# Performance work log

Hardware: AMD Instinct MI355X
Metric: run time of the kernel (lower is better)

Reference implementation:

```python
import jax, jax.numpy as jnp
import numpy as np
from jax import lax

T, B, INPUT, HID, OUT, FUT = 128, 1024, 4, 512, 4, 32


def setup_inputs() -> dict:
    key = jax.random.key(0)
    ks = jax.random.split(key, 12)
    s = 0.05  # small init like uniform(-1/sqrt(H), 1/sqrt(H))
    inp = {
        "x": jax.random.normal(ks[0], (T, B, INPUT), jnp.float32),
        "Wih1": jax.random.normal(ks[1], (4 * HID, INPUT), jnp.float32) * s,
        "Whh1": jax.random.normal(ks[2], (4 * HID, HID), jnp.float32) * s,
        "bih1": jax.random.normal(ks[3], (4 * HID,), jnp.float32) * s,
        "bhh1": jax.random.normal(ks[4], (4 * HID,), jnp.float32) * s,
        "Wih2": jax.random.normal(ks[5], (4 * HID, HID), jnp.float32) * s,
        "Whh2": jax.random.normal(ks[6], (4 * HID, HID), jnp.float32) * s,
        "bih2": jax.random.normal(ks[7], (4 * HID,), jnp.float32) * s,
        "bhh2": jax.random.normal(ks[8], (4 * HID,), jnp.float32) * s,
        "Wl": jax.random.normal(ks[9], (OUT, HID), jnp.float32) * s,
        "bl": jax.random.normal(ks[10], (OUT,), jnp.float32) * s,
        "future": FUT,
    }
    return inp


def _cell(xt, h, c, Wih, Whh, bih, bhh):
    # PyTorch LSTMCell gate order: i, f, g, o
    g = xt @ Wih.T + bih + h @ Whh.T + bhh  # [B, 4H]
    i, f, gg, o = jnp.split(g, 4, axis=-1)
    c = jax.nn.sigmoid(f) * c + jax.nn.sigmoid(i) * jnp.tanh(gg)
    h = jax.nn.sigmoid(o) * jnp.tanh(c)
    return h, c


def reference(x, Wih1, Whh1, bih1, bhh1, Wih2, Whh2, bih2, bhh2, Wl, bl, future):
    nb = x.shape[1]
    H = Whh1.shape[1]
    z = jnp.zeros((nb, H), x.dtype)

    def step1(carry, xt):
        h1, c1, h2, c2 = carry
        h1, c1 = _cell(xt, h1, c1, Wih1, Whh1, bih1, bhh1)
        h2, c2 = _cell(h1, h2, c2, Wih2, Whh2, bih2, bhh2)
        return (h1, c1, h2, c2), None

    (h1, c1, h2, c2), _ = lax.scan(step1, (z, z, z, z), x)
    tmp_out = h2  # frozen last hidden of cell 2 (faithful to original bug)

    def step2(carry, _):
        h1, c1, h2, c2 = carry
        # original future loop reuses lstm2 weights for both updates
        h1, c1 = _cell(tmp_out, h1, c1, Wih2, Whh2, bih2, bhh2)
        h2, c2 = _cell(h1, h2, c2, Wih2, Whh2, bih2, bhh2)
        out = h2 @ Wl.T + bl  # [B, OUT]
        return (h1, c1, h2, c2), out

    _, outs = lax.scan(step2, (h1, c1, h2, c2), None, length=future)
    return outs  # [future, B, OUT]
```

## Files before the change

kernel.cpp:

```cpp
#include <hip/hip_runtime.h>

typedef _Float16 v8h __attribute__((ext_vector_type(8)));
typedef float v4f __attribute__((ext_vector_type(4)));
typedef unsigned int uint;

#define OFF_BAR   0
#define OFF_AO0   4096
#define OFF_AO1   (OFF_AO0 + (1<<21))
#define OFF_AF0   (OFF_AO1 + (1<<21))
#define OFF_AF1   (OFF_AF0 + (1<<21))
#define OFF_W1    (OFF_AF1 + (1<<21))
#define OFF_W2    (OFF_W1 + (1<<21))
#define OFF_B1    (OFF_W2 + (1<<22))
#define OFF_B2    (OFF_B1 + 8192)

__global__ __launch_bounds__(256, 1)
void lstm_prep(const float* __restrict__ Whh1, const float* __restrict__ Wih2,
               const float* __restrict__ Whh2, const float* __restrict__ bih1,
               const float* __restrict__ bhh1, const float* __restrict__ bih2,
               const float* __restrict__ bhh2,
               _Float16* __restrict__ W1p, _Float16* __restrict__ W2p,
               float* __restrict__ bs1, float* __restrict__ bs2)
{
  const int total = 1048576 + 2097152 + 4096;
  for (int i = blockIdx.x*blockDim.x + threadIdx.x; i < total; i += gridDim.x*blockDim.x) {
    if (i < 1048576) {
      int nt = i >> 13, rem = i & 8191;
      int k32 = rem >> 9, c = rem & 511;
      int lane = c >> 3, el = c & 7;
      int n = nt*16 + (lane & 15);
      int k = k32*32 + (lane >> 4)*8 + el;
      W1p[i] = (_Float16)Whh1[n*512 + k];
    } else if (i < 3145728) {
      int j = i - 1048576;
      int nt = j >> 14, rem = j & 16383;
      int k32 = rem >> 9, c = rem & 511;
      int lane = c >> 3, el = c & 7;
      int n = nt*16 + (lane & 15);
      int k = k32*32 + (lane >> 4)*8 + el;
      float v = (k < 512) ? Wih2[n*512 + k] : Whh2[n*512 + (k - 512)];
      W2p[j] = (_Float16)v;
    } else {
      int n = i - 3145728;
      if (n < 2048) bs1[n] = bih1[n] + bhh1[n];
      else          bs2[n-2048] = bih2[n-2048] + bhh2[n-2048];
    }
  }
}

__device__ __forceinline__ float sigmoidf_(float z) { return 1.f / (1.f + __expf(-z)); }
__device__ __forceinline__ float tanhf_(float z)    { return 1.f - 2.f/(1.f + __expf(2.f*z)); }

__device__ __forceinline__ v8h ld_frag_dev(const _Float16* base, uint off) {
  union { unsigned long long u[2]; v8h h; } cv;
  const unsigned long long* q = (const unsigned long long*)(base + off);
  cv.u[0] = __hip_atomic_load(q,     __ATOMIC_RELAXED, __HIP_MEMORY_SCOPE_AGENT);
  cv.u[1] = __hip_atomic_load(q + 1, __ATOMIC_RELAXED, __HIP_MEMORY_SCOPE_AGENT);
  return cv.h;
}

__global__ __launch_bounds__(256, 2)
void lstm_main(const float* __restrict__ x, const float* __restrict__ Wih1,
               const float* __restrict__ Wl, const float* __restrict__ blv,
               _Float16* __restrict__ AO0, _Float16* __restrict__ AO1,
               _Float16* __restrict__ AF0, _Float16* __restrict__ AF1,
               const _Float16* __restrict__ W1, const _Float16* __restrict__ W2,
               const float* __restrict__ bs1, const float* __restrict__ bs2,
               int* __restrict__ bar, float* __restrict__ out)
{
  __shared__ float lred[14336];
  const int tid  = threadIdx.x;
  const int wv   = tid >> 6, lane = tid & 63;
  const int quad = lane >> 4, lc = lane & 15;
  const int kh   = wv >> 1;
  const int cw   = (wv & 1) ^ kh;
  const int bid  = blockIdx.x;
  const int jg   = bid >> 3;
  const int ht   = (bid & 7)*2 + (jg & 1);
  const int bt   = jg >> 1;

  _Float16* const AOv[2] = {AO0, AO1};
  _Float16* const AFv[2] = {AF0, AF1};

  const int erow = tid >> 3, enib = tid & 7;
  const int tid2  = tid - 128;
  const int b_loc = (tid2 >= 0) ? (tid2 >> 2) : 0, oct = tid2 & 3;
  const int m     = b_loc & 15, mtile_e = bt*2 + (b_loc >> 4);
  const int STASH = 8448;

  int ntg_[8];
  #pragma unroll
  for (int tt = 0; tt < 8; tt++) ntg_[tt] = (tt>>1)*32 + ht*2 + (tt&1);

  float c1s[4], c2s[4];
  #pragma unroll
  for (int i = 0; i < 4; i++) { c1s[i] = 0.f; c2s[i] = 0.f; }

  for (int r = 0; r < 162; r++) {
    const bool p1 = r < 129;
    const int  f  = r - 129;
    const int  wp = p1 ? (r & 1) : (f & 1);
    const int  rp = wp ^ 1;
    const _Float16* A1 = p1 ? AOv[rp] : AFv[rp];
    const _Float16* A2 = AOv[rp];
    const bool skip1 = (r == 128 || r == 161);
    const bool skip2 = (r == 0   || r == 129);

    const _Float16* Ac = cw ? A2 : A1;
    const _Float16* Bc = cw ? W2 : (p1 ? W1 : W2);
    const int wk   = cw ? 32 : (p1 ? 16 : 32);
    const int half = cw ? 16 : (p1 ? 8 : 16);
    const int ch0  = kh * half;

    v4f acc[2][8];
    #pragma unroll
    for (int i2 = 0; i2 < 2; i2++)
      #pragma unroll
      for (int tt = 0; tt < 8; tt++) acc[i2][tt] = (v4f){0,0,0,0};

    uint aoff[2];
    #pragma unroll
    for (int i2 = 0; i2 < 2; i2++)
      aoff[i2] = (uint)(((bt*2 + i2)*32 + ch0)*512 + lane*8);
    uint boff[8];
    #pragma unroll
    for (int tt = 0; tt < 8; tt++)
      boff[tt] = (uint)((ntg_[tt]*wk + ch0)*512 + lane*8);

    #pragma unroll 4
    for (int cc = 0; cc < half; cc++) {
      v8h av[2];
      #pragma unroll
      for (int i2 = 0; i2 < 2; i2++)
        av[i2] = ld_frag_dev(Ac, aoff[i2] + cc*512);
      #pragma unroll
      for (int tt = 0; tt < 8; tt++) {
        v8h bv = *(const v8h*)(Bc + boff[tt] + cc*512);
        #pragma unroll
        for (int i2 = 0; i2 < 2; i2++)
          acc[i2][tt] = __builtin_amdgcn_mfma_f32_16x16x32_f16(av[i2], bv, acc[i2][tt], 0, 0, 0);
      }
    }

    const int rbase = cw * 4096;
    if (kh) {
      #pragma unroll
      for (int i2 = 0; i2 < 2; i2++)
        #pragma unroll
        for (int tt = 0; tt < 8; tt++)
          *(v4f*)&lred[rbase + ((i2*8 + tt)*64 + lane)*4] = acc[i2][tt];
    }
    __syncthreads();
    if (!kh) {
      #pragma unroll
      for (int i2 = 0; i2 < 2; i2++)
        #pragma unroll
        for (int tt = 0; tt < 8; tt++)
          acc[i2][tt] += *(const v4f*)&lred[rbase + ((i2*8 + tt)*64 + lane)*4];
    }
    __syncthreads();

    if (!kh && cw == 0) {
      #pragma unroll
      for (int i2 = 0; i2 < 2; i2++)
        #pragma unroll
        for (int tt = 0; tt < 8; tt++) {
          int row = i2*16 + quad*4;
          int col = tt*16 + lc;
          #pragma unroll
          for (int rr = 0; rr < 4; rr++) lred[(row + rr)*132 + col] = acc[i2][tt][rr];
        }
    }
    __syncthreads();

    {
      const float* bsx = p1 ? bs1 : bs2;
      float g[4][4];
      #pragma unroll
      for (int g4 = 0; g4 < 4; g4++) {
        v4f gv = *(const v4f*)&lred[erow*132 + g4*32 + enib*4];
        v4f bv = *(const v4f*)&bsx[g4*512 + ht*32 + enib*4];
        #pragma unroll
        for (int j = 0; j < 4; j++) g[g4][j] = gv[j] + bv[j];
      }
      if (p1 && r < 128) {
        const v4f xv = *(const v4f*)(x + ((size_t)r*1024 + bt*32 + erow)*4);
        #pragma unroll
        for (int g4 = 0; g4 < 4; g4++)
          #pragma unroll
          for (int j = 0; j < 4; j++) {
            int hh = ht*32 + enib*4 + j;
            const v4f w = *(const v4f*)(Wih1 + (size_t)(g4*512 + hh)*4);
            g[g4][j] += xv[0]*w[0] + xv[1]*w[1] + xv[2]*w[2] + xv[3]*w[3];
          }
      }
      if (!skip1) {
        v4f hf;
        #pragma unroll
        for (int j = 0; j < 4; j++) {
          float ig = sigmoidf_(g[0][j]), fg = sigmoidf_(g[1][j]);
          float gg = tanhf_(g[2][j]),    og = sigmoidf_(g[3][j]);
          float c = fg*c1s[j] + ig*gg;
          c1s[j] = c;
          hf[j] = og * tanhf_(c);
        }
        *(v4f*)&lred[STASH + erow*36 + enib*4] = hf;
      }
    }
    __syncthreads();

    if (tid >= 128 && !skip1) {
      v4f h0 = *(const v4f*)&lred[STASH + b_loc*36 + oct*8];
      v4f h1 = *(const v4f*)&lred[STASH + b_loc*36 + oct*8 + 4];
      union { _Float16 h8[8]; unsigned long long u[2]; } hu;
      #pragma unroll
      for (int j = 0; j < 4; j++) { hu.h8[j] = (_Float16)h0[j]; hu.h8[4+j] = (_Float16)h1[j]; }
      auto st16 = [&](_Float16* bp, int chunk) {
        unsigned long long* p = (unsigned long long*)
          (bp + (((size_t)(mtile_e*32 + chunk)) << 9) + (oct*16 + m)*8);
        __hip_atomic_store(p,     hu.u[0], __ATOMIC_RELAXED, __HIP_MEMORY_SCOPE_AGENT);
        __hip_atomic_store(p + 1, hu.u[1], __ATOMIC_RELAXED, __HIP_MEMORY_SCOPE_AGENT);
      };
      if (p1) {
        st16(AOv[wp], ht);
        if (r == 127) st16(AFv[1], 16 + ht);
      } else {
        st16(AFv[wp], 16 + ht);
        st16(AOv[wp], ht);
      }
    }
    if (!kh && cw == 1) {
      #pragma unroll
      for (int i2 = 0; i2 < 2; i2++)
        #pragma unroll
        for (int tt = 0; tt < 8; tt++) {
          int row = i2*16 + quad*4;
          int col = tt*16 + lc;
          #pragma unroll
          for (int rr = 0; rr < 4; rr++) lred[(row + rr)*132 + col] = acc[i2][tt][rr];
        }
    }
    __syncthreads();

    {
      float g[4][4];
      #pragma unroll
      for (int g4 = 0; g4 < 4; g4++) {
        v4f gv = *(const v4f*)&lred[erow*132 + g4*32 + enib*4];
        v4f bv = *(const v4f*)&bs2[g4*512 + ht*32 + enib*4];
        #pragma unroll
        for (int j = 0; j < 4; j++) g[g4][j] = gv[j] + bv[j];
      }
      if (!skip2) {
        v4f hf;
        #pragma unroll
        for (int j = 0; j < 4; j++) {
          float ig = sigmoidf_(g[0][j]), fg = sigmoidf_(g[1][j]);
          float gg = tanhf_(g[2][j]),    og = sigmoidf_(g[3][j]);
          float c = fg*c2s[j] + ig*gg;
          c2s[j] = c;
          hf[j] = og * tanhf_(c);
        }
        *(v4f*)&lred[STASH + erow*36 + enib*4] = hf;
      }
    }
    __syncthreads();

    if (tid >= 128 && !skip2) {
      v4f h0 = *(const v4f*)&lred[STASH + b_loc*36 + oct*8];
      v4f h1 = *(const v4f*)&lred[STASH + b_loc*36 + oct*8 + 4];
      union { _Float16 h8[8]; unsigned long long u[2]; } hu;
      #pragma unroll
      for (int j = 0; j < 4; j++) { hu.h8[j] = (_Float16)h0[j]; hu.h8[4+j] = (_Float16)h1[j]; }
      auto st16 = [&](_Float16* bp, int chunk) {
        unsigned long long* p = (unsigned long long*)
          (bp + (((size_t)(mtile_e*32 + chunk)) << 9) + (oct*16 + m)*8);
        __hip_atomic_store(p,     hu.u[0], __ATOMIC_RELAXED, __HIP_MEMORY_SCOPE_AGENT);
        __hip_atomic_store(p + 1, hu.u[1], __ATOMIC_RELAXED, __HIP_MEMORY_SCOPE_AGENT);
      };
      st16(AOv[wp], 16 + ht);
      if (r == 128) { st16(AFv[0], ht); st16(AFv[1], ht); }
    }
    if (tid < 128 && !p1 && r >= 130) {
      const int s = r - 130;
      int bb = tid >> 2, o = tid & 3;
      float sa = (ht == 0) ? blv[o] : 0.f;
      const float* wl = Wl + (size_t)o*512 + ht*32;
      #pragma unroll
      for (int jj = 0; jj < 32; jj++) sa += lred[STASH + bb*36 + jj] * wl[jj];
      atomicAdd(&out[(((size_t)s*1024) + bt*32 + bb)*4 + o], sa);
    }
    __syncthreads();

    if (tid == 0) {
      int* ctr = bar + bt*32;
      __hip_atomic_fetch_add(ctr, 1, __ATOMIC_RELAXED, __HIP_MEMORY_SCOPE_AGENT);
      const int target = 16*(r+1);
      while (__hip_atomic_load(ctr, __ATOMIC_RELAXED, __HIP_MEMORY_SCOPE_AGENT) < target)
        __builtin_amdgcn_s_sleep(1);
    }
    __syncthreads();
  }
}

extern "C" void kernel_launch(void* const* d_in, const int* in_sizes, int n_in,
                              void* d_out, int out_size, void* d_ws, size_t ws_size,
                              hipStream_t stream) {
  const float* x    = (const float*)d_in[0];
  const float* Wih1 = (const float*)d_in[1];
  const float* Whh1 = (const float*)d_in[2];
  const float* bih1 = (const float*)d_in[3];
  const float* bhh1 = (const float*)d_in[4];
  const float* Wih2 = (const float*)d_in[5];
  const float* Whh2 = (const float*)d_in[6];
  const float* bih2 = (const float*)d_in[7];
  const float* bhh2 = (const float*)d_in[8];
  const float* Wl   = (const float*)d_in[9];
  const float* bl   = (const float*)d_in[10];

  char* ws = (char*)d_ws;
  int*      bar = (int*)(ws + OFF_BAR);
  _Float16* AO0 = (_Float16*)(ws + OFF_AO0);
  _Float16* AO1 = (_Float16*)(ws + OFF_AO1);
  _Float16* AF0 = (_Float16*)(ws + OFF_AF0);
  _Float16* AF1 = (_Float16*)(ws + OFF_AF1);
  _Float16* W1p = (_Float16*)(ws + OFF_W1);
  _Float16* W2p = (_Float16*)(ws + OFF_W2);
  float*    bs1 = (float*)(ws + OFF_B1);
  float*    bs2 = (float*)(ws + OFF_B2);

  hipMemsetAsync(ws, 0, (size_t)OFF_W1, stream);
  hipMemsetAsync(d_out, 0, (size_t)out_size * sizeof(float), stream);

  lstm_prep<<<2048, 256, 0, stream>>>(Whh1, Wih2, Whh2, bih1, bhh1, bih2, bhh2,
                                      W1p, W2p, bs1, bs2);
  lstm_main<<<512, 256, 0, stream>>>(x, Wih1, Wl, bl, AO0, AO1, AF0, AF1,
                                     W1p, W2p, bs1, bs2, bar, (float*)d_out);
}
```

Baseline: 2.916 ms.

## Software-pipeline A-fragment loads and signal barrier before output projection

Replaces the inner GEMM loop with a templated, fully unrolled version. It prefetches up to eight K-chunks of the recurrent A fragments into registers ahead of use, to hide global/L2 latency on the atomic loads. It also moves the barrier arrival to before the output-projection atomicAdd work, so other blocks can proceed while this block computes its output contribution. The cost is higher register pressure from the prefetch buffer, which may reduce occupancy or cause spills.

```diff
diff --git a/kernel.cpp b/kernel.cpp
--- a/kernel.cpp
+++ b/kernel.cpp
@@ -59,6 +59,36 @@
   return cv.h;
 }
 
+template<int HALF>
+__device__ __forceinline__ void gemm_k(const _Float16* __restrict__ Ac,
+                                       const _Float16* __restrict__ Bc,
+                                       const uint* aoff, const uint* boff,
+                                       v4f (&acc)[2][8])
+{
+  constexpr int PF = (HALF < 8) ? HALF : 8;
+  v8h apf[PF][2];
+  #pragma unroll
+  for (int s = 0; s < PF; s++) {
+    apf[s][0] = ld_frag_dev(Ac, aoff[0] + s*512);
+    apf[s][1] = ld_frag_dev(Ac, aoff[1] + s*512);
+  }
+  #pragma unroll
+  for (int cc = 0; cc < HALF; cc++) {
+    v8h av0 = apf[cc % PF][0];
+    v8h av1 = apf[cc % PF][1];
+    if (cc + PF < HALF) {
+      apf[cc % PF][0] = ld_frag_dev(Ac, aoff[0] + (cc + PF)*512);
+      apf[cc % PF][1] = ld_frag_dev(Ac, aoff[1] + (cc + PF)*512);
+    }
+    #pragma unroll
+    for (int tt = 0; tt < 8; tt++) {
+      v8h bv = *(const v8h*)(Bc + boff[tt] + cc*512);
+      acc[0][tt] = __builtin_amdgcn_mfma_f32_16x16x32_f16(av0, bv, acc[0][tt], 0, 0, 0);
+      acc[1][tt] = __builtin_amdgcn_mfma_f32_16x16x32_f16(av1, bv, acc[1][tt], 0, 0, 0);
+    }
+  }
+}
+
 __global__ __launch_bounds__(256, 2)
 void lstm_main(const float* __restrict__ x, const float* __restrict__ Wih1,
                const float* __restrict__ Wl, const float* __restrict__ blv,
@@ -127,20 +157,8 @@
     for (int tt = 0; tt < 8; tt++)
       boff[tt] = (uint)((ntg_[tt]*wk + ch0)*512 + lane*8);
 
-    #pragma unroll 4
-    for (int cc = 0; cc < half; cc++) {
-      v8h av[2];
-      #pragma unroll
-      for (int i2 = 0; i2 < 2; i2++)
-        av[i2] = ld_frag_dev(Ac, aoff[i2] + cc*512);
-      #pragma unroll
-      for (int tt = 0; tt < 8; tt++) {
-        v8h bv = *(const v8h*)(Bc + boff[tt] + cc*512);
-        #pragma unroll
-        for (int i2 = 0; i2 < 2; i2++)
-          acc[i2][tt] = __builtin_amdgcn_mfma_f32_16x16x32_f16(av[i2], bv, acc[i2][tt], 0, 0, 0);
-      }
-    }
+    if (half == 8) gemm_k<8>(Ac, Bc, aoff, boff, acc);
+    else           gemm_k<16>(Ac, Bc, aoff, boff, acc);
 
     const int rbase = cw * 4096;
     if (kh) {
@@ -281,6 +299,12 @@
       st16(AOv[wp], 16 + ht);
       if (r == 128) { st16(AFv[0], ht); st16(AFv[1], ht); }
     }
+    __syncthreads();
+
+    if (tid == 0) {
+      int* ctr = bar + bt*32;
+      __hip_atomic_fetch_add(ctr, 1, __ATOMIC_RELAXED, __HIP_MEMORY_SCOPE_AGENT);
+    }
     if (tid < 128 && !p1 && r >= 130) {
       const int s = r - 130;
       int bb = tid >> 2, o = tid & 3;
@@ -290,11 +314,8 @@
       for (int jj = 0; jj < 32; jj++) sa += lred[STASH + bb*36 + jj] * wl[jj];
       atomicAdd(&out[(((size_t)s*1024) + bt*32 + bb)*4 + o], sa);
     }
-    __syncthreads();
-
     if (tid == 0) {
       int* ctr = bar + bt*32;
-      __hip_atomic_fetch_add(ctr, 1, __ATOMIC_RELAXED, __HIP_MEMORY_SCOPE_AGENT);
       const int target = 16*(r+1);
       while (__hip_atomic_load(ctr, __ATOMIC_RELAXED, __HIP_MEMORY_SCOPE_AGENT) < target)
         __builtin_amdgcn_s_sleep(1);
```

After: 3.624 ms. 24.3% more time.

## Process both LSTM cells' epilogues concurrently with split thread halves

Applied to the files above, without the earlier changes.

The split-K reduction now adds partial sums straight into the gate tiles in shared memory, so the separate reduction buffer pass goes away. Both cells' gate tiles (cw 0 and 1) are written to separate regions. The two halves of the block then run the cell-1 and cell-2 nonlinearities in parallel, each thread handling 8 hidden units. This removes several __syncthreads barriers and serialized epilogue phases per step, in exchange for more registers per thread (8 cell states, g[4][8]) and a larger shared footprint.

```diff
diff --git a/kernel.cpp b/kernel.cpp
--- a/kernel.cpp
+++ b/kernel.cpp
@@ -50,6 +50,7 @@
 
 __device__ __forceinline__ float sigmoidf_(float z) { return 1.f / (1.f + __expf(-z)); }
 __device__ __forceinline__ float tanhf_(float z)    { return 1.f - 2.f/(1.f + __expf(2.f*z)); }
+__device__ __forceinline__ float dot4_(v4f a, v4f b){ return a[0]*b[0]+a[1]*b[1]+a[2]*b[2]+a[3]*b[3]; }
 
 __device__ __forceinline__ v8h ld_frag_dev(const _Float16* base, uint off) {
   union { unsigned long long u[2]; v8h h; } cv;
@@ -82,19 +83,22 @@
   _Float16* const AOv[2] = {AO0, AO1};
   _Float16* const AFv[2] = {AF0, AF1};
 
-  const int erow = tid >> 3, enib = tid & 7;
+  const int half2 = tid >> 7;
+  const int et    = tid & 127;
+  const int erow2 = et >> 2;
+  const int ecg   = et & 3;
   const int tid2  = tid - 128;
   const int b_loc = (tid2 >= 0) ? (tid2 >> 2) : 0, oct = tid2 & 3;
   const int m     = b_loc & 15, mtile_e = bt*2 + (b_loc >> 4);
-  const int STASH = 8448;
+  const int GR1 = 0, GR2 = 4224, ST1 = 8448, ST2 = 9600;
 
   int ntg_[8];
   #pragma unroll
   for (int tt = 0; tt < 8; tt++) ntg_[tt] = (tt>>1)*32 + ht*2 + (tt&1);
 
-  float c1s[4], c2s[4];
+  float cs[8];
   #pragma unroll
-  for (int i = 0; i < 4; i++) { c1s[i] = 0.f; c2s[i] = 0.f; }
+  for (int i = 0; i < 8; i++) cs[i] = 0.f;
 
   for (int r = 0; r < 162; r++) {
     const bool p1 = r < 129;
@@ -142,25 +146,8 @@
       }
     }
 
-    const int rbase = cw * 4096;
+    const int gbase = cw ? GR2 : GR1;
     if (kh) {
-      #pragma unroll
-      for (int i2 = 0; i2 < 2; i2++)
-        #pragma unroll
-        for (int tt = 0; tt < 8; tt++)
-          *(v4f*)&lred[rbase + ((i2*8 + tt)*64 + lane)*4] = acc[i2][tt];
-    }
-    __syncthreads();
-    if (!kh) {
-      #pragma unroll
-      for (int i2 = 0; i2 < 2; i2++)
-        #pragma unroll
-        for (int tt = 0; tt < 8; tt++)
-          acc[i2][tt] += *(const v4f*)&lred[rbase + ((i2*8 + tt)*64 + lane)*4];
-    }
-    __syncthreads();
-
-    if (!kh && cw == 0) {
       #pragma unroll
       for (int i2 = 0; i2 < 2; i2++)
         #pragma unroll
@@ -168,118 +155,100 @@
           int row = i2*16 + quad*4;
           int col = tt*16 + lc;
           #pragma unroll
-          for (int rr = 0; rr < 4; rr++) lred[(row + rr)*132 + col] = acc[i2][tt][rr];
+          for (int rr = 0; rr < 4; rr++) lred[(row + rr)*132 + gbase + col] = acc[i2][tt][rr];
         }
     }
     __syncthreads();
 
+    if (!kh) {
+      #pragma unroll
+      for (int i2 = 0; i2 < 2; i2++)
+        #pragma unroll
+        for (int tt = 0; tt < 8; tt++) {
+          int row = i2*16 + quad*4;
+          int col = tt*16 + lc;
+          #pragma unroll
+          for (int rr = 0; rr < 4; rr++) {
+            int p = (row + rr)*132 + gbase + col;
+            lred[p] = acc[i2][tt][rr] + lred[p];
+          }
+        }
+    }
+    __syncthreads();
+
     {
-      const float* bsx = p1 ? bs1 : bs2;
-      float g[4][4];
+      const int gb = half2 ? GR2 : GR1;
+      const int sb = half2 ? ST2 : ST1;
+      const float* bsx = half2 ? bs2 : (p1 ? bs1 : bs2);
+      const bool skipc = half2 ? skip2 : skip1;
+      const bool xterm = (half2 == 0) && p1 && (r < 128);
+      float g[4][8];
       #pragma unroll
       for (int g4 = 0; g4 < 4; g4++) {
-        v4f gv = *(const v4f*)&lred[erow*132 + g4*32 + enib*4];
-        v4f bv = *(const v4f*)&bsx[g4*512 + ht*32 + enib*4];
-        #pragma unroll
-        for (int j = 0; j < 4; j++) g[g4][j] = gv[j] + bv[j];
-      }
-      if (p1 && r < 128) {
-        const v4f xv = *(const v4f*)(x + ((size_t)r*1024 + bt*32 + erow)*4);
+        v4f a0 = *(const v4f*)&lred[gb + erow2*132 + g4*32 + ecg*8];
+        v4f a1 = *(const v4f*)&lred[gb + erow2*132 + g4*32 + ecg*8 + 4];
+        v4f b0 = *(const v4f*)&bsx[g4*512 + ht*32 + ecg*8];
+        v4f b1 = *(const v4f*)&bsx[g4*512 + ht*32 + ecg*8 + 4];
+        #pragma unroll
+        for (int j = 0; j < 4; j++) { g[g4][j] = a0[j] + b0[j]; g[g4][4+j] = a1[j] + b1[j]; }
+      }
+      if (xterm) {
+        const v4f xv = *(const v4f*)(x + ((size_t)r*1024 + bt*32 + erow2)*4);
         #pragma unroll
         for (int g4 = 0; g4 < 4; g4++)
           #pragma unroll
-          for (int j = 0; j < 4; j++) {
-            int hh = ht*32 + enib*4 + j;
+          for (int j = 0; j < 8; j++) {
+            int hh = ht*32 + ecg*8 + j;
             const v4f w = *(const v4f*)(Wih1 + (size_t)(g4*512 + hh)*4);
-            g[g4][j] += xv[0]*w[0] + xv[1]*w[1] + xv[2]*w[2] + xv[3]*w[3];
+            g[g4][j] += dot4_(xv, w);
           }
       }
-      if (!skip1) {
-        v4f hf;
-        #pragma unroll
-        for (int j = 0; j < 4; j++) {
+      if (!skipc) {
+        v4f h0, h1v;
+        #pragma unroll
+        for (int j = 0; j < 8; j++) {
           float ig = sigmoidf_(g[0][j]), fg = sigmoidf_(g[1][j]);
           float gg = tanhf_(g[2][j]),    og = sigmoidf_(g[3][j]);
-          float c = fg*c1s[j] + ig*gg;
-          c1s[j] = c;
-          hf[j] = og * tanhf_(c);
+          float c = fg*cs[j] + ig*gg;
+          cs[j] = c;
+          float hv = og * tanhf_(c);
+          if (j < 4) h0[j] = hv; else h1v[j-4] = hv;
         }
-        *(v4f*)&lred[STASH + erow*36 + enib*4] = hf;
-      }
-    }
-    __syncthreads();
-
-    if (tid >= 128 && !skip1) {
-      v4f h0 = *(const v4f*)&lred[STASH + b_loc*36 + oct*8];
-      v4f h1 = *(const v4f*)&lred[STASH + b_loc*36 + oct*8 + 4];
+        *(v4f*)&lred[sb + erow2*36 + ecg*8]     = h0;
+        *(v4f*)&lred[sb + erow2*36 + ecg*8 + 4] = h1v;
+      }
+    }
+    __syncthreads();
+
+    if (tid >= 128) {
       union { _Float16 h8[8]; unsigned long long u[2]; } hu;
-      #pragma unroll
-      for (int j = 0; j < 4; j++) { hu.h8[j] = (_Float16)h0[j]; hu.h8[4+j] = (_Float16)h1[j]; }
       auto st16 = [&](_Float16* bp, int chunk) {
         unsigned long long* p = (unsigned long long*)
           (bp + (((size_t)(mtile_e*32 + chunk)) << 9) + (oct*16 + m)*8);
         __hip_atomic_store(p,     hu.u[0], __ATOMIC_RELAXED, __HIP_MEMORY_SCOPE_AGENT);
         __hip_atomic_store(p + 1, hu.u[1], __ATOMIC_RELAXED, __HIP_MEMORY_SCOPE_AGENT);
       };
-      if (p1) {
-        st16(AOv[wp], ht);
-        if (r == 127) st16(AFv[1], 16 + ht);
-      } else {
-        st16(AFv[wp], 16 + ht);
-        st16(AOv[wp], ht);
-      }
-    }
-    if (!kh && cw == 1) {
-      #pragma unroll
-      for (int i2 = 0; i2 < 2; i2++)
-        #pragma unroll
-        for (int tt = 0; tt < 8; tt++) {
-          int row = i2*16 + quad*4;
-          int col = tt*16 + lc;
-          #pragma unroll
-          for (int rr = 0; rr < 4; rr++) lred[(row + rr)*132 + col] = acc[i2][tt][rr];
+      if (!skip1) {
+        v4f h0 = *(const v4f*)&lred[ST1 + b_loc*36 + oct*8];
+        v4f h1v = *(const v4f*)&lred[ST1 + b_loc*36 + oct*8 + 4];
+        #pragma unroll
+        for (int j = 0; j < 4; j++) { hu.h8[j] = (_Float16)h0[j]; hu.h8[4+j] = (_Float16)h1v[j]; }
+        if (p1) {
+          st16(AOv[wp], ht);
+          if (r == 127) st16(AFv[1], 16 + ht);
+        } else {
+          st16(AFv[wp], 16 + ht);
+          st16(AOv[wp], ht);
         }
-    }
-    __syncthreads();
-
-    {
-      float g[4][4];
-      #pragma unroll
-      for (int g4 = 0; g4 < 4; g4++) {
-        v4f gv = *(const v4f*)&lred[erow*132 + g4*32 + enib*4];
-        v4f bv = *(const v4f*)&bs2[g4*512 + ht*32 + enib*4];
-        #pragma unroll
-        for (int j = 0; j < 4; j++) g[g4][j] = gv[j] + bv[j];
       }
       if (!skip2) {
-        v4f hf;
-        #pragma unroll
-        for (int j = 0; j < 4; j++) {
-          float ig = sigmoidf_(g[0][j]), fg = sigmoidf_(g[1][j]);
-          float gg = tanhf_(g[2][j]),    og = sigmoidf_(g[3][j]);
-          float c = fg*c2s[j] + ig*gg;
-          c2s[j] = c;
-          hf[j] = og * tanhf_(c);
-        }
-        *(v4f*)&lred[STASH + erow*36 + enib*4] = hf;
-      }
-    }
-    __syncthreads();
-
-    if (tid >= 128 && !skip2) {
-      v4f h0 = *(const v4f*)&lred[STASH + b_loc*36 + oct*8];
-      v4f h1 = *(const v4f*)&lred[STASH + b_loc*36 + oct*8 + 4];
-      union { _Float16 h8[8]; unsigned long long u[2]; } hu;
-      #pragma unroll
-      for (int j = 0; j < 4; j++) { hu.h8[j] = (_Float16)h0[j]; hu.h8[4+j] = (_Float16)h1[j]; }
-      auto st16 = [&](_Float16* bp, int chunk) {
-        unsigned long long* p = (unsigned long long*)
-          (bp + (((size_t)(mtile_e*32 + chunk)) << 9) + (oct*16 + m)*8);
-        __hip_atomic_store(p,     hu.u[0], __ATOMIC_RELAXED, __HIP_MEMORY_SCOPE_AGENT);
-        __hip_atomic_store(p + 1, hu.u[1], __ATOMIC_RELAXED, __HIP_MEMORY_SCOPE_AGENT);
-      };
-      st16(AOv[wp], 16 + ht);
-      if (r == 128) { st16(AFv[0], ht); st16(AFv[1], ht); }
+        v4f h0 = *(const v4f*)&lred[ST2 + b_loc*36 + oct*8];
+        v4f h1v = *(const v4f*)&lred[ST2 + b_loc*36 + oct*8 + 4];
+        #pragma unroll
+        for (int j = 0; j < 4; j++) { hu.h8[j] = (_Float16)h0[j]; hu.h8[4+j] = (_Float16)h1v[j]; }
+        st16(AOv[wp], 16 + ht);
+        if (r == 128) { st16(AFv[0], ht); st16(AFv[1], ht); }
+      }
     }
     if (tid < 128 && !p1 && r >= 130) {
       const int s = r - 130;
@@ -287,7 +256,7 @@
       float sa = (ht == 0) ? blv[o] : 0.f;
       const float* wl = Wl + (size_t)o*512 + ht*32;
       #pragma unroll
-      for (int jj = 0; jj < 32; jj++) sa += lred[STASH + bb*36 + jj] * wl[jj];
+      for (int jj = 0; jj < 32; jj++) sa += lred[ST2 + bb*36 + jj] * wl[jj];
       atomicAdd(&out[(((size_t)s*1024) + bt*32 + bb)*4 + o], sa);
     }
     __syncthreads();
```

Result: slower. 3.101 ms (+6.3%).

## Split hidden tiles in half and run twice as many persistent blocks

Applied to the files above, without the earlier changes.

Each block now computes 16 hidden units (4 gate n-tiles) instead of 32. The grid grows from 512 to 1024 blocks, with launch bounds raised to 4 blocks per CU and LDS shrunk so they stay co-resident. The aim is to shorten the per-step MFMA and weight-load chain on the recurrent critical path. The cost is that each block reloads the same activation fragments, and the software grid barrier now waits on 32 blocks per batch tile instead of 16. It also relies on all 1024 blocks being resident at once.

```diff
diff --git a/kernel.cpp b/kernel.cpp
--- a/kernel.cpp
+++ b/kernel.cpp
@@ -50,6 +50,7 @@
 
 __device__ __forceinline__ float sigmoidf_(float z) { return 1.f / (1.f + __expf(-z)); }
 __device__ __forceinline__ float tanhf_(float z)    { return 1.f - 2.f/(1.f + __expf(2.f*z)); }
+__device__ __forceinline__ float dot4_(v4f a, v4f b){ return a[0]*b[0]+a[1]*b[1]+a[2]*b[2]+a[3]*b[3]; }
 
 __device__ __forceinline__ v8h ld_frag_dev(const _Float16* base, uint off) {
   union { unsigned long long u[2]; v8h h; } cv;
@@ -59,7 +60,7 @@
   return cv.h;
 }
 
-__global__ __launch_bounds__(256, 2)
+__global__ __launch_bounds__(256, 4)
 void lstm_main(const float* __restrict__ x, const float* __restrict__ Wih1,
                const float* __restrict__ Wl, const float* __restrict__ blv,
                _Float16* __restrict__ AO0, _Float16* __restrict__ AO1,
@@ -68,7 +69,7 @@
                const float* __restrict__ bs1, const float* __restrict__ bs2,
                int* __restrict__ bar, float* __restrict__ out)
 {
-  __shared__ float lred[14336];
+  __shared__ float lred[10112];
   const int tid  = threadIdx.x;
   const int wv   = tid >> 6, lane = tid & 63;
   const int quad = lane >> 4, lc = lane & 15;
@@ -76,25 +77,27 @@
   const int cw   = (wv & 1) ^ kh;
   const int bid  = blockIdx.x;
   const int jg   = bid >> 3;
-  const int ht   = (bid & 7)*2 + (jg & 1);
-  const int bt   = jg >> 1;
+  const int ht   = (bid & 7)*4 + (jg & 3);
+  const int bt   = jg >> 2;
+  const int chv  = ht & 1, chk = ht >> 1;
 
   _Float16* const AOv[2] = {AO0, AO1};
   _Float16* const AFv[2] = {AF0, AF1};
 
-  const int erow = tid >> 3, enib = tid & 7;
+  const int erow = tid >> 3, ec = tid & 7;
   const int tid2  = tid - 128;
-  const int b_loc = (tid2 >= 0) ? (tid2 >> 2) : 0, oct = tid2 & 3;
+  const int b_loc = (tid2 >= 0) ? (tid2 >> 1) & 31 : 0, octl = tid2 & 1;
+  const int oct   = chv*2 + octl;
   const int m     = b_loc & 15, mtile_e = bt*2 + (b_loc >> 4);
-  const int STASH = 8448;
-
-  int ntg_[8];
+  const int GR = 4096, ST = 6272;
+
+  int ntg_[4];
   #pragma unroll
-  for (int tt = 0; tt < 8; tt++) ntg_[tt] = (tt>>1)*32 + ht*2 + (tt&1);
-
-  float c1s[4], c2s[4];
+  for (int tt = 0; tt < 4; tt++) ntg_[tt] = tt*32 + ht;
+
+  float c1s[2], c2s[2];
   #pragma unroll
-  for (int i = 0; i < 4; i++) { c1s[i] = 0.f; c2s[i] = 0.f; }
+  for (int i = 0; i < 2; i++) { c1s[i] = 0.f; c2s[i] = 0.f; }
 
   for (int r = 0; r < 162; r++) {
     const bool p1 = r < 129;
@@ -112,19 +115,19 @@
     const int half = cw ? 16 : (p1 ? 8 : 16);
     const int ch0  = kh * half;
 
-    v4f acc[2][8];
+    v4f acc[2][4];
     #pragma unroll
     for (int i2 = 0; i2 < 2; i2++)
       #pragma unroll
-      for (int tt = 0; tt < 8; tt++) acc[i2][tt] = (v4f){0,0,0,0};
+      for (int tt = 0; tt < 4; tt++) acc[i2][tt] = (v4f){0,0,0,0};
 
     uint aoff[2];
     #pragma unroll
     for (int i2 = 0; i2 < 2; i2++)
       aoff[i2] = (uint)(((bt*2 + i2)*32 + ch0)*512 + lane*8);
-    uint boff[8];
+    uint boff[4];
     #pragma unroll
-    for (int tt = 0; tt < 8; tt++)
+    for (int tt = 0; tt < 4; tt++)
       boff[tt] = (uint)((ntg_[tt]*wk + ch0)*512 + lane*8);
 
     #pragma unroll 4
@@ -134,7 +137,7 @@
       for (int i2 = 0; i2 < 2; i2++)
         av[i2] = ld_frag_dev(Ac, aoff[i2] + cc*512);
       #pragma unroll
-      for (int tt = 0; tt < 8; tt++) {
+      for (int tt = 0; tt < 4; tt++) {
         v8h bv = *(const v8h*)(Bc + boff[tt] + cc*512);
         #pragma unroll
         for (int i2 = 0; i2 < 2; i2++)
@@ -142,21 +145,21 @@
       }
     }
 
-    const int rbase = cw * 4096;
+    const int rbase = cw * 2048;
     if (kh) {
       #pragma unroll
       for (int i2 = 0; i2 < 2; i2++)
         #pragma unroll
-        for (int tt = 0; tt < 8; tt++)
-          *(v4f*)&lred[rbase + ((i2*8 + tt)*64 + lane)*4] = acc[i2][tt];
+        for (int tt = 0; tt < 4; tt++)
+          *(v4f*)&lred[rbase + ((i2*4 + tt)*64 + lane)*4] = acc[i2][tt];
     }
     __syncthreads();
     if (!kh) {
       #pragma unroll
       for (int i2 = 0; i2 < 2; i2++)
         #pragma unroll
-        for (int tt = 0; tt < 8; tt++)
-          acc[i2][tt] += *(const v4f*)&lred[rbase + ((i2*8 + tt)*64 + lane)*4];
+        for (int tt = 0; tt < 4; tt++)
+          acc[i2][tt] += *(const v4f*)&lred[rbase + ((i2*4 + tt)*64 + lane)*4];
     }
     __syncthreads();
 
@@ -164,54 +167,52 @@
       #pragma unroll
       for (int i2 = 0; i2 < 2; i2++)
         #pragma unroll
-        for (int tt = 0; tt < 8; tt++) {
+        for (int tt = 0; tt < 4; tt++) {
           int row = i2*16 + quad*4;
           int col = tt*16 + lc;
           #pragma unroll
-          for (int rr = 0; rr < 4; rr++) lred[(row + rr)*132 + col] = acc[i2][tt][rr];
+          for (int rr = 0; rr < 4; rr++) lred[GR + (row + rr)*68 + col] = acc[i2][tt][rr];
         }
     }
     __syncthreads();
 
     {
       const float* bsx = p1 ? bs1 : bs2;
-      float g[4][4];
+      float g[4][2];
       #pragma unroll
       for (int g4 = 0; g4 < 4; g4++) {
-        v4f gv = *(const v4f*)&lred[erow*132 + g4*32 + enib*4];
-        v4f bv = *(const v4f*)&bsx[g4*512 + ht*32 + enib*4];
-        #pragma unroll
-        for (int j = 0; j < 4; j++) g[g4][j] = gv[j] + bv[j];
+        #pragma unroll
+        for (int j = 0; j < 2; j++)
+          g[g4][j] = lred[GR + erow*68 + g4*16 + ec*2 + j]
+                   + bsx[g4*512 + ht*16 + ec*2 + j];
       }
       if (p1 && r < 128) {
         const v4f xv = *(const v4f*)(x + ((size_t)r*1024 + bt*32 + erow)*4);
         #pragma unroll
         for (int g4 = 0; g4 < 4; g4++)
           #pragma unroll
-          for (int j = 0; j < 4; j++) {
-            int hh = ht*32 + enib*4 + j;
+          for (int j = 0; j < 2; j++) {
+            int hh = ht*16 + ec*2 + j;
             const v4f w = *(const v4f*)(Wih1 + (size_t)(g4*512 + hh)*4);
-            g[g4][j] += xv[0]*w[0] + xv[1]*w[1] + xv[2]*w[2] + xv[3]*w[3];
+            g[g4][j] += dot4_(xv, w);
           }
       }
       if (!skip1) {
-        v4f hf;
-        #pragma unroll
-        for (int j = 0; j < 4; j++) {
+        #pragma unroll
+        for (int j = 0; j < 2; j++) {
           float ig = sigmoidf_(g[0][j]), fg = sigmoidf_(g[1][j]);
           float gg = tanhf_(g[2][j]),    og = sigmoidf_(g[3][j]);
           float c = fg*c1s[j] + ig*gg;
           c1s[j] = c;
-          hf[j] = og * tanhf_(c);
+          lred[ST + erow*20 + ec*2 + j] = og * tanhf_(c);
         }
-        *(v4f*)&lred[STASH + erow*36 + enib*4] = hf;
-      }
-    }
-    __syncthreads();
-
-    if (tid >= 128 && !skip1) {
-      v4f h0 = *(const v4f*)&lred[STASH + b_loc*36 + oct*8];
-      v4f h1 = *(const v4f*)&lred[STASH + b_loc*36 + oct*8 + 4];
+      }
+    }
+    __syncthreads();
+
+    if (tid2 >= 0 && tid2 < 64 && !skip1) {
+      v4f h0 = *(const v4f*)&lred[ST + b_loc*20 + octl*8];
+      v4f h1 = *(const v4f*)&lred[ST + b_loc*20 + octl*8 + 4];
       union { _Float16 h8[8]; unsigned long long u[2]; } hu;
       #pragma unroll
       for (int j = 0; j < 4; j++) { hu.h8[j] = (_Float16)h0[j]; hu.h8[4+j] = (_Float16)h1[j]; }
@@ -222,53 +223,51 @@
         __hip_atomic_store(p + 1, hu.u[1], __ATOMIC_RELAXED, __HIP_MEMORY_SCOPE_AGENT);
       };
       if (p1) {
-        st16(AOv[wp], ht);
-        if (r == 127) st16(AFv[1], 16 + ht);
+        st16(AOv[wp], chk);
+        if (r == 127) st16(AFv[1], 16 + chk);
       } else {
-        st16(AFv[wp], 16 + ht);
-        st16(AOv[wp], ht);
+        st16(AFv[wp], 16 + chk);
+        st16(AOv[wp], chk);
       }
     }
     if (!kh && cw == 1) {
       #pragma unroll
       for (int i2 = 0; i2 < 2; i2++)
         #pragma unroll
-        for (int tt = 0; tt < 8; tt++) {
+        for (int tt = 0; tt < 4; tt++) {
           int row = i2*16 + quad*4;
           int col = tt*16 + lc;
           #pragma unroll
-          for (int rr = 0; rr < 4; rr++) lred[(row + rr)*132 + col] = acc[i2][tt][rr];
+          for (int rr = 0; rr < 4; rr++) lred[GR + (row + rr)*68 + col] = acc[i2][tt][rr];
         }
     }
     __syncthreads();
 
     {
-      float g[4][4];
+      float g[4][2];
       #pragma unroll
       for (int g4 = 0; g4 < 4; g4++) {
-        v4f gv = *(const v4f*)&lred[erow*132 + g4*32 + enib*4];
-        v4f bv = *(const v4f*)&bs2[g4*512 + ht*32 + enib*4];
-        #pragma unroll
-        for (int j = 0; j < 4; j++) g[g4][j] = gv[j] + bv[j];
+        #pragma unroll
+        for (int j = 0; j < 2; j++)
+          g[g4][j] = lred[GR + erow*68 + g4*16 + ec*2 + j]
+                   + bs2[g4*512 + ht*16 + ec*2 + j];
       }
       if (!skip2) {
-        v4f hf;
-        #pragma unroll
-        for (int j = 0; j < 4; j++) {
+        #pragma unroll
+        for (int j = 0; j < 2; j++) {
           float ig = sigmoidf_(g[0][j]), fg = sigmoidf_(g[1][j]);
           float gg = tanhf_(g[2][j]),    og = sigmoidf_(g[3][j]);
           float c = fg*c2s[j] + ig*gg;
           c2s[j] = c;
-          hf[j] = og * tanhf_(c);
+          lred[ST + erow*20 + ec*2 + j] = og * tanhf_(c);
         }
-        *(v4f*)&lred[STASH + erow*36 + enib*4] = hf;
-      }
-    }
-    __syncthreads();
-
-    if (tid >= 128 && !skip2) {
-      v4f h0 = *(const v4f*)&lred[STASH + b_loc*36 + oct*8];
-      v4f h1 = *(const v4f*)&lred[STASH + b_loc*36 + oct*8 + 4];
+      }
+    }
+    __syncthreads();
+
+    if (tid2 >= 0 && tid2 < 64 && !skip2) {
+      v4f h0 = *(const v4f*)&lred[ST + b_loc*20 + octl*8];
+      v4f h1 = *(const v4f*)&lred[ST + b_loc*20 + octl*8 + 4];
       union { _Float16 h8[8]; unsigned long long u[2]; } hu;
       #pragma unroll
       for (int j = 0; j < 4; j++) { hu.h8[j] = (_Float16)h0[j]; hu.h8[4+j] = (_Float16)h1[j]; }
@@ -278,16 +277,16 @@
         __hip_atomic_store(p,     hu.u[0], __ATOMIC_RELAXED, __HIP_MEMORY_SCOPE_AGENT);
         __hip_atomic_store(p + 1, hu.u[1], __ATOMIC_RELAXED, __HIP_MEMORY_SCOPE_AGENT);
       };
-      st16(AOv[wp], 16 + ht);
-      if (r == 128) { st16(AFv[0], ht); st16(AFv[1], ht); }
+      st16(AOv[wp], 16 + chk);
+      if (r == 128) { st16(AFv[0], chk); st16(AFv[1], chk); }
     }
     if (tid < 128 && !p1 && r >= 130) {
       const int s = r - 130;
       int bb = tid >> 2, o = tid & 3;
       float sa = (ht == 0) ? blv[o] : 0.f;
-      const float* wl = Wl + (size_t)o*512 + ht*32;
-      #pragma unroll
-      for (int jj = 0; jj < 32; jj++) sa += lred[STASH + bb*36 + jj] * wl[jj];
+      const float* wl = Wl + (size_t)o*512 + ht*16;
+      #pragma unroll
+      for (int jj = 0; jj < 16; jj++) sa += lred[ST + bb*20 + jj] * wl[jj];
       atomicAdd(&out[(((size_t)s*1024) + bt*32 + bb)*4 + o], sa);
     }
     __syncthreads();
@@ -295,7 +294,7 @@
     if (tid == 0) {
       int* ctr = bar + bt*32;
       __hip_atomic_fetch_add(ctr, 1, __ATOMIC_RELAXED, __HIP_MEMORY_SCOPE_AGENT);
-      const int target = 16*(r+1);
+      const int target = 32*(r+1);
       while (__hip_atomic_load(ctr, __ATOMIC_RELAXED, __HIP_MEMORY_SCOPE_AGENT) < target)
         __builtin_amdgcn_s_sleep(1);
     }
@@ -334,6 +333,6 @@
 
   lstm_prep<<<2048, 256, 0, stream>>>(Whh1, Wih2, Whh2, bih1, bhh1, bih2, bhh2,
                                       W1p, W2p, bs1, bs2);
-  lstm_main<<<512, 256, 0, stream>>>(x, Wih1, Wl, bl, AO0, AO1, AF0, AF1,
-                                     W1p, W2p, bs1, bs2, bar, (float*)d_out);
+  lstm_main<<<1024, 256, 0, stream>>>(x, Wih1, Wl, bl, AO0, AO1, AF0, AF1,
+                                      W1p, W2p, bs1, bs2, bar, (float*)d_out);
 }
```

Measured after the change: 4.748 ms. 62.8% more time.
